# Optimization experiments

Hardware: AMD Instinct MI355X
Metric: run time of the kernel (lower is better)

The kernel has to match this reference:

```python
import jax, jax.numpy as jnp
import numpy as np

B, N, C, F = 64, 64, 8, 256      # batch, neighbors per sample, in_channels, in_features
OC, OF = 8, 256                  # out_channels, out_features


def setup_inputs() -> dict:
    key = jax.random.key(0)
    k0, k1, k2, k3, k4 = jax.random.split(key, 5)
    x = jax.random.normal(k0, (B, C, F), dtype=jnp.float32)
    neighbor = jax.random.normal(k1, (B, N, C, F), dtype=jnp.float32)
    # att1/att2: nn.Linear(in_features, in_channels, bias=False) -> weight (C, F)
    W1 = jax.random.normal(k2, (C, F), dtype=jnp.float32) * (1.0 / np.sqrt(F))
    W2 = jax.random.normal(k3, (C, F), dtype=jnp.float32) * (1.0 / np.sqrt(F))
    # conv: nn.Conv1d(C, OC*OF, kernel_size=F, bias=False) -> weight (OC*OF, C, F)
    Wc = jax.random.normal(k4, (OC * OF, C, F), dtype=jnp.float32) * (1.0 / np.sqrt(C * F))
    return {"x": x, "neighbor": neighbor, "W1": W1, "W2": W2, "Wc": Wc}


def _sgnroot(a):
    return jnp.sign(a) * jnp.sqrt(jnp.clip(jnp.abs(a), 1e-8))


def _row_normalize(a):
    # torch: x / (x.abs().sum(1, keepdim=True) + 1e-7); dim 1 is the channel dim of (B,C,F,F)
    a = a / (jnp.abs(a).sum(axis=1, keepdims=True) + 1e-7)
    return jnp.where(jnp.isnan(a), 0.0, a)


def _feature_adjacency(x, neighbor, W1, W2):
    # w[b,n] = sum_{c,k} (x[b] @ W1^T)[c,k] * sum_{k,l} (neighbor[b,n] @ W2^T)[k,l]
    s1 = jnp.einsum('bcf,kf->b', x, W1)            # total sum of att1(x[b])
    s2 = jnp.einsum('bncf,kf->bn', neighbor, W2)   # total sum of att2(y[b,n])
    w = s1[:, None] * s2                            # (B, N)
    # fadj[b,c,a,d] = sum_n x[b,c,a] * neighbor[b,n,c,d] * w[b,n]
    fadj = jnp.einsum('bca,bncd,bn->bcad', x, neighbor, w)
    fadj = fadj + jnp.swapaxes(fadj, -2, -1)
    return _row_normalize(_sgnroot(fadj))


def _conv_transform(z, Wc, lead_shape):
    # Conv1d(C, OC*OF, kernel_size=F, bias=False) over (.., C, F) == full contraction
    out = jnp.einsum('...cf,ocf->...o', z, Wc)
    return out.reshape(*lead_shape, OC, OF)


def reference(x, neighbor, W1, W2, Wc):
    adj = _feature_adjacency(x, neighbor, W1, W2)              # (B,C,F,F)
    # transform(x, adj): (adj @ x.unsqueeze(-1)).squeeze(-1) then conv
    zx = jnp.einsum('bcad,bcd->bca', adj, x)                   # (B,C,F)
    x_out = _conv_transform(zx, Wc, (x.shape[0],))             # (B,OC,OF)
    # transform(neighbor[i], adj[i:i+1]) for each i -> adj broadcasts over N
    zn = jnp.einsum('bcad,bncd->bnca', adj, neighbor)          # (B,N,C,F)
    n_out = _conv_transform(zn, Wc, (x.shape[0], neighbor.shape[1]))  # (B,N,OC,OF)
    return x_out, n_out
```

## Files before the change

kernel.cpp:

```cpp
#include <hip/hip_runtime.h>
#include <hip/hip_bf16.h>
#include <math.h>

#define B_ 64
#define N_ 64
#define C_ 8
#define F_ 256
#define K_ 2048
#define NO_ 2048
#define M_TOT 4160

typedef __attribute__((ext_vector_type(8))) short bf16x8;
typedef __attribute__((ext_vector_type(4))) float f32x4;

__global__ __launch_bounds__(256) void sums_wc_k(const float* __restrict__ x,
        const float* __restrict__ nb, const float* __restrict__ W1,
        const float* __restrict__ W2, const float* __restrict__ Wc,
        float* __restrict__ s1, float* __restrict__ s2,
        __hip_bfloat16* __restrict__ Bbuf) {
    int blk = blockIdx.x;
    int f = threadIdx.x;
    if (blk >= B_ * N_ + B_) {
        int i = (blk - (B_ * N_ + B_)) * 1024 + f * 4;
        float4 v = *(const float4*)(Wc + i);
        Bbuf[i + 0] = __float2bfloat16(v.x);
        Bbuf[i + 1] = __float2bfloat16(v.y);
        Bbuf[i + 2] = __float2bfloat16(v.z);
        Bbuf[i + 3] = __float2bfloat16(v.w);
        return;
    }
    float val;
    if (blk < B_ * N_) {
        const float* base = nb + (size_t)blk * (C_ * F_);
        float wsum = 0.f;
        #pragma unroll
        for (int k = 0; k < C_; ++k) wsum += W2[k * F_ + f];
        float cs = 0.f;
        #pragma unroll
        for (int c = 0; c < C_; ++c) cs += base[c * F_ + f];
        val = cs * wsum;
    } else {
        int b = blk - B_ * N_;
        const float* base = x + (size_t)b * (C_ * F_);
        float wsum = 0.f;
        #pragma unroll
        for (int k = 0; k < C_; ++k) wsum += W1[k * F_ + f];
        float cs = 0.f;
        #pragma unroll
        for (int c = 0; c < C_; ++c) cs += base[c * F_ + f];
        val = cs * wsum;
    }
    #pragma unroll
    for (int off = 32; off > 0; off >>= 1) val += __shfl_down(val, off, 64);
    __shared__ float wred[4];
    int w = f >> 6;
    if ((f & 63) == 0) wred[w] = val;
    __syncthreads();
    if (f == 0) {
        float s = wred[0] + wred[1] + wred[2] + wred[3];
        if (blk < B_ * N_) s2[blk] = s;
        else s1[blk - B_ * N_] = s;
    }
}

__global__ __launch_bounds__(1024) void t_k(const float* __restrict__ nb,
        const float* __restrict__ s1, const float* __restrict__ s2,
        float* __restrict__ t) {
    int blk = blockIdx.x;
    int b = blk / C_, c = blk % C_;
    int tid = threadIdx.x;
    int q = tid >> 8, d = tid & 255;
    const float* p = nb + ((size_t)(b * N_) * C_ + c) * F_ + d;
    const float* s2p = s2 + b * N_;
    float acc = 0.f;
    #pragma unroll
    for (int j = 0; j < 16; ++j) {
        int n = q * 16 + j;
        acc += p[(size_t)n * C_ * F_] * s2p[n];
    }
    __shared__ float part[4][F_];
    part[q][d] = acc;
    __syncthreads();
    if (tid < 256) {
        float s = part[0][d] + part[1][d] + part[2][d] + part[3][d];
        t[(size_t)blk * F_ + d] = s * s1[b];
    }
}

__global__ __launch_bounds__(256) void denom_k(const float* __restrict__ x,
        const float* __restrict__ t, float* __restrict__ rdenom) {
    int blk = blockIdx.x;
    int b = blk >> 8, a = blk & 255;
    int d = threadIdx.x;
    float acc = 1e-7f;
    #pragma unroll
    for (int c = 0; c < C_; ++c) {
        size_t o = ((size_t)b * C_ + c) * F_;
        float xa = x[o + a], ta = t[o + a];
        float xd = x[o + d], td = t[o + d];
        float v = xa * td + xd * ta;
        float r = __builtin_amdgcn_sqrtf(fmaxf(fabsf(v), 1e-8f));
        acc += (v != 0.f) ? r : 0.f;
    }
    rdenom[(size_t)blk * F_ + d] = __builtin_amdgcn_rcpf(acc);
}

__device__ __forceinline__ float sgnroot_dev(float v) {
    float r = __builtin_amdgcn_sqrtf(fmaxf(fabsf(v), 1e-8f));
    return (v > 0.f) ? r : ((v < 0.f) ? -r : 0.f);
}

#define ZNX_PAD 264
__global__ __launch_bounds__(256) void znx_k(const float* __restrict__ x,
        const float* __restrict__ t, const float* __restrict__ rdenom,
        const float* __restrict__ nb, __hip_bfloat16* __restrict__ Abuf) {
    int bc = blockIdx.x;
    int b = bc >> 3, c = bc & 7;
    int tid = threadIdx.x;
    int wave = tid >> 6, lane = tid & 63;
    __shared__ float xs[F_], ts[F_];
    __shared__ __hip_bfloat16 nbB[80 * ZNX_PAD];

    xs[tid] = x[(size_t)bc * F_ + tid];
    ts[tid] = t[(size_t)bc * F_ + tid];
    {
        int r = tid >> 2, cs0 = (tid & 3) * 64;
        const float* src = nb + (((size_t)(b * N_ + r)) * C_ + c) * F_ + cs0;
        __hip_bfloat16* dst = nbB + r * ZNX_PAD + cs0;
        #pragma unroll
        for (int j = 0; j < 64; j += 4) {
            float4 v = *(const float4*)(src + j);
            dst[j + 0] = __float2bfloat16(v.x);
            dst[j + 1] = __float2bfloat16(v.y);
            dst[j + 2] = __float2bfloat16(v.z);
            dst[j + 3] = __float2bfloat16(v.w);
        }
    }
    if (tid < 64) {
        float4 v = *(const float4*)(x + (size_t)bc * F_ + tid * 4);
        __hip_bfloat16* dst = nbB + 64 * ZNX_PAD + tid * 4;
        dst[0] = __float2bfloat16(v.x);
        dst[1] = __float2bfloat16(v.y);
        dst[2] = __float2bfloat16(v.z);
        dst[3] = __float2bfloat16(v.w);
    }
    {
        __hip_bfloat16 z = __float2bfloat16(0.f);
        #pragma unroll
        for (int j = 0; j < 16; ++j) {
            int o = 65 * ZNX_PAD + tid * 16 + j;
            if (o < 80 * ZNX_PAD) nbB[o] = z;
        }
    }
    __syncthreads();

    const int aq = lane & 15;
    const int dq = lane >> 4;
    #pragma unroll
    for (int atile = 0; atile < 4; ++atile) {
        int a = wave * 64 + atile * 16 + aq;
        float xa = xs[a], ta = ts[a];
        const float* drow = rdenom + ((size_t)b * F_ + a) * F_;
        f32x4 acc[5] = {};
        #pragma unroll
        for (int kc = 0; kc < 8; ++kc) {
            int d0 = kc * 32 + dq * 8;
            float4 xv0 = *(const float4*)(xs + d0);
            float4 xv1 = *(const float4*)(xs + d0 + 4);
            float4 tv0 = *(const float4*)(ts + d0);
            float4 tv1 = *(const float4*)(ts + d0 + 4);
            float4 dn0 = *(const float4*)(drow + d0);
            float4 dn1 = *(const float4*)(drow + d0 + 4);
            float xv[8] = {xv0.x, xv0.y, xv0.z, xv0.w, xv1.x, xv1.y, xv1.z, xv1.w};
            float tv[8] = {tv0.x, tv0.y, tv0.z, tv0.w, tv1.x, tv1.y, tv1.z, tv1.w};
            float dn[8] = {dn0.x, dn0.y, dn0.z, dn0.w, dn1.x, dn1.y, dn1.z, dn1.w};
            union { bf16x8 v; __hip_bfloat16 h[8]; } bu;
            #pragma unroll
            for (int j = 0; j < 8; ++j) {
                float g = sgnroot_dev(xa * tv[j] + xv[j] * ta);
                bu.h[j] = __float2bfloat16(g * dn[j]);
            }
            #pragma unroll
            for (int mt = 0; mt < 5; ++mt) {
                bf16x8 af = *(const bf16x8*)(nbB + (mt * 16 + aq) * ZNX_PAD
                                             + kc * 32 + dq * 8);
                acc[mt] = __builtin_amdgcn_mfma_f32_16x16x32_bf16(
                    af, bu.v, acc[mt], 0, 0, 0);
            }
        }
        int colA = c * F_ + a;
        #pragma unroll
        for (int mt = 0; mt < 4; ++mt) {
            int row = 64 + b * N_ + mt * 16 + dq * 4;
            #pragma unroll
            for (int i = 0; i < 4; ++i)
                Abuf[(size_t)(row + i) * K_ + colA] = __float2bfloat16(acc[mt][i]);
        }
        if (dq == 0)
            Abuf[(size_t)b * K_ + colA] = __float2bfloat16(acc[4][0]);
    }
}

__global__ __launch_bounds__(256) void gemm_bf16_k(
        const __hip_bfloat16* __restrict__ A,
        const __hip_bfloat16* __restrict__ Bm,
        float* __restrict__ Cm) {
    __shared__ char lds[49152] __attribute__((aligned(16)));
    const int t = threadIdx.x;
    const int wave = t >> 6;
    const int lane = t & 63;
    const int col0 = blockIdx.x * 128;
    const int row0 = blockIdx.y * 128;
    const int wrow0 = (wave & 1) * 64;
    const int wcol0 = (wave >> 1) * 64;
    const int aq = lane & 15;
    const int dq = lane >> 4;

    const int rA0 = t >> 2;
    const int kcs = ((t & 3) - ((t >> 3) & 3)) & 3;
    const int kc = kcs * 8;
    const int grA0 = min(row0 + rA0, M_TOT - 1);
    const int grA1 = min(row0 + rA0 + 64, M_TOT - 1);
    const int gcB0 = col0 + rA0;
    const int gcB1 = col0 + rA0 + 64;
    const size_t aoff0 = (size_t)grA0 * K_ + kc;
    const size_t aoff1 = (size_t)grA1 * K_ + kc;
    const size_t boff0 = (size_t)gcB0 * K_ + kc;
    const size_t boff1 = (size_t)gcB1 * K_ + kc;
    const int swz = ((dq + (aq >> 1)) & 3) * 16;
    const int ldsw = wave * 1024;

    f32x4 acc[4][4] = {};

#define STAGE(BI, TK) do {                                                     \
    const int k0_ = (TK) * 32;                                                 \
    char* la_ = lds + (BI) * 16384 + ldsw;                                     \
    char* lb_ = la_ + 8192;                                                    \
    __builtin_amdgcn_global_load_lds(                                          \
        (const __attribute__((address_space(1))) void*)(A + aoff0 + k0_),      \
        (__attribute__((address_space(3))) void*)la_, 16, 0, 0);               \
    __builtin_amdgcn_global_load_lds(                                          \
        (const __attribute__((address_space(1))) void*)(A + aoff1 + k0_),      \
        (__attribute__((address_space(3))) void*)(la_ + 4096), 16, 0, 0);      \
    __builtin_amdgcn_global_load_lds(                                          \
        (const __attribute__((address_space(1))) void*)(Bm + boff0 + k0_),     \
        (__attribute__((address_space(3))) void*)lb_, 16, 0, 0);               \
    __builtin_amdgcn_global_load_lds(                                          \
        (const __attribute__((address_space(1))) void*)(Bm + boff1 + k0_),     \
        (__attribute__((address_space(3))) void*)(lb_ + 4096), 16, 0, 0);      \
} while (0)

#define COMPUTE(BI) do {                                                       \
    const char* la_ = lds + (BI) * 16384;                                      \
    const char* lb_ = la_ + 8192;                                              \
    bf16x8 af_[4], bf_[4];                                                     \
    _Pragma("unroll")                                                          \
    for (int rb = 0; rb < 4; ++rb)                                             \
        af_[rb] = *(const bf16x8*)(la_ + (wrow0 + rb * 16 + aq) * 64 + swz);   \
    _Pragma("unroll")                                                          \
    for (int cb = 0; cb < 4; ++cb)                                             \
        bf_[cb] = *(const bf16x8*)(lb_ + (wcol0 + cb * 16 + aq) * 64 + swz);   \
    _Pragma("unroll")                                                          \
    for (int rb = 0; rb < 4; ++rb)                                             \
        _Pragma("unroll")                                                      \
        for (int cb = 0; cb < 4; ++cb)                                         \
            acc[rb][cb] = __builtin_amdgcn_mfma_f32_16x16x32_bf16(             \
                af_[rb], bf_[cb], acc[rb][cb], 0, 0, 0);                       \
} while (0)

#define WAIT_PIPE(N) do {                                                      \
    asm volatile("s_waitcnt vmcnt(" #N ")" ::: "memory");                      \
    __builtin_amdgcn_sched_barrier(0);                                         \
    __builtin_amdgcn_s_barrier();                                              \
    __builtin_amdgcn_sched_barrier(0);                                         \
} while (0)

    STAGE(0, 0);
    STAGE(1, 1);
    STAGE(2, 2);

    for (int t3 = 0; t3 < 60; t3 += 3) {
        WAIT_PIPE(8);
        COMPUTE(0);
        __builtin_amdgcn_s_barrier();
        STAGE(0, t3 + 3);

        WAIT_PIPE(8);
        COMPUTE(1);
        __builtin_amdgcn_s_barrier();
        STAGE(1, t3 + 4);

        WAIT_PIPE(8);
        COMPUTE(2);
        __builtin_amdgcn_s_barrier();
        STAGE(2, t3 + 5);
    }
    WAIT_PIPE(8);
    COMPUTE(0);
    __builtin_amdgcn_s_barrier();
    STAGE(0, 63);
    WAIT_PIPE(8);
    COMPUTE(1);
    WAIT_PIPE(4);
    COMPUTE(2);
    WAIT_PIPE(0);
    COMPUTE(0);

#undef STAGE
#undef COMPUTE
#undef WAIT_PIPE

    #pragma unroll
    for (int rb = 0; rb < 4; ++rb) {
        int rowbase = row0 + wrow0 + rb * 16 + (lane >> 4) * 4;
        #pragma unroll
        for (int cb = 0; cb < 4; ++cb) {
            int col = col0 + wcol0 + cb * 16 + (lane & 15);
            #pragma unroll
            for (int i = 0; i < 4; ++i) {
                int row = rowbase + i;
                if (row < M_TOT)
                    Cm[(size_t)row * NO_ + col] = acc[rb][cb][i];
            }
        }
    }
}

extern "C" void kernel_launch(void* const* d_in, const int* in_sizes, int n_in,
                              void* d_out, int out_size, void* d_ws, size_t ws_size,
                              hipStream_t stream) {
    const float* x  = (const float*)d_in[0];
    const float* nb = (const float*)d_in[1];
    const float* W1 = (const float*)d_in[2];
    const float* W2 = (const float*)d_in[3];
    const float* Wc = (const float*)d_in[4];
    float* out = (float*)d_out;
    float* ws = (float*)d_ws;

    float* s1    = ws;
    float* s2    = ws + 64;
    float* t     = ws + 4160;
    float* rden  = ws + 135232;
    __hip_bfloat16* Abuf = (__hip_bfloat16*)(ws + 4329536);
    __hip_bfloat16* Bbuf = Abuf + (size_t)M_TOT * K_;

    hipLaunchKernelGGL(sums_wc_k, dim3(B_ * N_ + B_ + (K_ * NO_) / 1024),
                       dim3(256), 0, stream, x, nb, W1, W2, Wc, s1, s2, Bbuf);
    hipLaunchKernelGGL(t_k, dim3(B_ * C_), dim3(1024), 0, stream, nb, s1, s2, t);
    hipLaunchKernelGGL(denom_k, dim3(B_ * F_), dim3(256), 0, stream, x, t, rden);
    hipLaunchKernelGGL(znx_k, dim3(B_ * C_), dim3(256), 0, stream,
                       x, t, rden, nb, Abuf);
    hipLaunchKernelGGL(gemm_bf16_k, dim3(16, 33), dim3(256), 0, stream,
                       Abuf, Bbuf, out);
}
```

Baseline: 207.7 us.

## Stage znx output through LDS for coalesced stores, vectorize bf16 conversions, add setprio

```diff
diff --git a/kernel.cpp b/kernel.cpp
--- a/kernel.cpp
+++ b/kernel.cpp
@@ -12,6 +12,12 @@
 
 typedef __attribute__((ext_vector_type(8))) short bf16x8;
 typedef __attribute__((ext_vector_type(4))) float f32x4;
+
+__device__ __forceinline__ unsigned short bfbits(float f) {
+    union { __hip_bfloat16 h; unsigned short u; } cv;
+    cv.h = __float2bfloat16(f);
+    return cv.u;
+}
 
 __global__ __launch_bounds__(256) void sums_wc_k(const float* __restrict__ x,
         const float* __restrict__ nb, const float* __restrict__ W1,
@@ -23,10 +29,8 @@
     if (blk >= B_ * N_ + B_) {
         int i = (blk - (B_ * N_ + B_)) * 1024 + f * 4;
         float4 v = *(const float4*)(Wc + i);
-        Bbuf[i + 0] = __float2bfloat16(v.x);
-        Bbuf[i + 1] = __float2bfloat16(v.y);
-        Bbuf[i + 2] = __float2bfloat16(v.z);
-        Bbuf[i + 3] = __float2bfloat16(v.w);
+        ushort4 u = { bfbits(v.x), bfbits(v.y), bfbits(v.z), bfbits(v.w) };
+        *(ushort4*)(&Bbuf[i]) = u;
         return;
     }
     float val;
@@ -111,7 +115,7 @@
 }
 
 #define ZNX_PAD 264
-__global__ __launch_bounds__(256) void znx_k(const float* __restrict__ x,
+__global__ __launch_bounds__(256, 2) void znx_k(const float* __restrict__ x,
         const float* __restrict__ t, const float* __restrict__ rdenom,
         const float* __restrict__ nb, __hip_bfloat16* __restrict__ Abuf) {
     int bc = blockIdx.x;
@@ -130,19 +134,14 @@
         #pragma unroll
         for (int j = 0; j < 64; j += 4) {
             float4 v = *(const float4*)(src + j);
-            dst[j + 0] = __float2bfloat16(v.x);
-            dst[j + 1] = __float2bfloat16(v.y);
-            dst[j + 2] = __float2bfloat16(v.z);
-            dst[j + 3] = __float2bfloat16(v.w);
+            ushort4 u = { bfbits(v.x), bfbits(v.y), bfbits(v.z), bfbits(v.w) };
+            *(ushort4*)(&dst[j]) = u;
         }
     }
     if (tid < 64) {
         float4 v = *(const float4*)(x + (size_t)bc * F_ + tid * 4);
-        __hip_bfloat16* dst = nbB + 64 * ZNX_PAD + tid * 4;
-        dst[0] = __float2bfloat16(v.x);
-        dst[1] = __float2bfloat16(v.y);
-        dst[2] = __float2bfloat16(v.z);
-        dst[3] = __float2bfloat16(v.w);
+        ushort4 u = { bfbits(v.x), bfbits(v.y), bfbits(v.z), bfbits(v.w) };
+        *(ushort4*)(&nbB[64 * ZNX_PAD + tid * 4]) = u;
     }
     {
         __hip_bfloat16 z = __float2bfloat16(0.f);
@@ -156,12 +155,12 @@
 
     const int aq = lane & 15;
     const int dq = lane >> 4;
+    f32x4 acc[4][5] = {};
     #pragma unroll
     for (int atile = 0; atile < 4; ++atile) {
         int a = wave * 64 + atile * 16 + aq;
         float xa = xs[a], ta = ts[a];
         const float* drow = rdenom + ((size_t)b * F_ + a) * F_;
-        f32x4 acc[5] = {};
         #pragma unroll
         for (int kc = 0; kc < 8; ++kc) {
             int d0 = kc * 32 + dq * 8;
@@ -184,20 +183,37 @@
             for (int mt = 0; mt < 5; ++mt) {
                 bf16x8 af = *(const bf16x8*)(nbB + (mt * 16 + aq) * ZNX_PAD
                                              + kc * 32 + dq * 8);
-                acc[mt] = __builtin_amdgcn_mfma_f32_16x16x32_bf16(
-                    af, bu.v, acc[mt], 0, 0, 0);
+                acc[atile][mt] = __builtin_amdgcn_mfma_f32_16x16x32_bf16(
+                    af, bu.v, acc[atile][mt], 0, 0, 0);
             }
         }
-        int colA = c * F_ + a;
+    }
+
+    __syncthreads();
+    #pragma unroll
+    for (int atile = 0; atile < 4; ++atile) {
+        int a = wave * 64 + atile * 16 + aq;
         #pragma unroll
         for (int mt = 0; mt < 4; ++mt) {
-            int row = 64 + b * N_ + mt * 16 + dq * 4;
             #pragma unroll
-            for (int i = 0; i < 4; ++i)
-                Abuf[(size_t)(row + i) * K_ + colA] = __float2bfloat16(acc[mt][i]);
+            for (int i = 0; i < 4; ++i) {
+                int n = mt * 16 + dq * 4 + i;
+                nbB[n * ZNX_PAD + a] = __float2bfloat16(acc[atile][mt][i]);
+            }
         }
         if (dq == 0)
-            Abuf[(size_t)b * K_ + colA] = __float2bfloat16(acc[4][0]);
+            nbB[64 * ZNX_PAD + a] = __float2bfloat16(acc[atile][4][0]);
+    }
+    __syncthreads();
+    for (int it = 0; it < 17; ++it) {
+        int q = it * 256 + tid;
+        if (q < 4160) {
+            int row = q >> 6;
+            int off = (q & 63) * 4;
+            ushort4 u = *(const ushort4*)(&nbB[row * ZNX_PAD + off]);
+            int grow = (row < 64) ? (64 + b * N_ + row) : b;
+            *(ushort4*)(&Abuf[(size_t)grow * K_ + c * F_ + off]) = u;
+        }
     }
 }
 
@@ -260,12 +276,14 @@
     _Pragma("unroll")                                                          \
     for (int cb = 0; cb < 4; ++cb)                                             \
         bf_[cb] = *(const bf16x8*)(lb_ + (wcol0 + cb * 16 + aq) * 64 + swz);   \
+    __builtin_amdgcn_s_setprio(1);                                             \
     _Pragma("unroll")                                                          \
     for (int rb = 0; rb < 4; ++rb)                                             \
         _Pragma("unroll")                                                      \
         for (int cb = 0; cb < 4; ++cb)                                         \
             acc[rb][cb] = __builtin_amdgcn_mfma_f32_16x16x32_bf16(             \
                 af_[rb], bf_[cb], acc[rb][cb], 0, 0, 0);                       \
+    __builtin_amdgcn_s_setprio(0);                                             \
 } while (0)
 
 #define WAIT_PIPE(N) do {                                                      \
```

Measured after the change: 209.3 us. No clear change (+0.8%).
